# Kernel tuning notes

Hardware: AMD Instinct MI355X
Metric: run time of the kernel (lower is better)

## Reference

```python
import jax, jax.numpy as jnp
import numpy as np


def _fracdiff(X, alpha):
    """Fractional differencing (1-L)^alpha applied per batch/channel.
    X: (B, T, n), alpha: (B, n) >= 0. Weights w_0 = 1, w_k = w_{k-1}*(k-1-alpha)/k.
    Y[b, t, i] = sum_{k=0..t} w[b, k, i] * X[b, t-k, i]  (causal filter).
    Computed as a linear convolution via FFT (same math, O(T log T)).
    """
    B, T, n = X.shape
    k = jnp.arange(1, T, dtype=X.dtype)[None, :, None]          # (1, T-1, 1)
    factors = (k - 1.0 - alpha[:, None, :]) / k                  # (B, T-1, n)
    w = jnp.concatenate(
        [jnp.ones((B, 1, n), X.dtype), jnp.cumprod(factors, axis=1)], axis=1
    )                                                            # (B, T, n)
    L = 2 * T  # zero-pad to avoid circular wrap-around
    Xf = jnp.fft.rfft(X, n=L, axis=1)
    Wf = jnp.fft.rfft(w, n=L, axis=1)
    Y = jnp.fft.irfft(Xf * Wf, n=L, axis=1)[:, :T, :]
    return Y.astype(X.dtype)


def setup_inputs() -> dict:
    key = jax.random.key(0)
    kx, ka, kA = jax.random.split(key, 3)
    B, T, n = 8, 8192, 128
    X = jax.random.normal(kx, (B, T, n), dtype=jnp.float32)
    # normalize per trial/channel, mirroring normalize_data=True in __init__
    X = (X - X.mean(axis=1, keepdims=True)) / X.std(axis=1, keepdims=True, ddof=1)
    alpha = jax.random.uniform(ka, (B, n), dtype=jnp.float32)
    A = jax.random.normal(kA, (B, n, n), dtype=jnp.float32) * 0.1
    return {"X": X, "alpha": alpha, "A": A}


def reference(X, alpha, A):
    # _resid(): Y = fracdiff(X, relu(alpha)); E = Y[:,1:,:] - X[:,:-1,:] @ A^T
    Y = _fracdiff(X, jax.nn.relu(alpha))
    Yhat = jnp.einsum('bti,bji->btj', X[:, :-1, :], A)  # bmm(X, A.transpose(1,2))
    return Y[:, 1:, :] - Yhat
```

## Files before the change

### kernel.cpp

```cpp
#include <hip/hip_runtime.h>

#define T 8192
#define NCH 128
#define NB 8
#define NS (NB * NCH)
#define TM1 (T - 1)

typedef __bf16 v8bf __attribute__((ext_vector_type(8)));
typedef float v16f __attribute__((ext_vector_type(16)));

#define WREV_LEN 8448
#define WREV_COPY_STRIDE ((size_t)NS * WREV_LEN)

#define ILIM_TRUNC 144
#define KCHUNKS 19
#define WR_D_MIN 2880
#define KMAX_W 2559
#define NW 2560

struct __attribute__((packed, aligned(4))) U16 { uint4 v; };
struct __attribute__((packed, aligned(4))) F16V { float4 v; };

__device__ __forceinline__ uint bf_bits(float f) {
  union { float f; uint u; } v; v.f = f;
  return (v.u + 0x7FFFu + ((v.u >> 16) & 1u)) >> 16;
}

__device__ __forceinline__ uint wbits(const float* wsh, int k) {
  if ((unsigned)k > (unsigned)KMAX_W) return 0u;
  return bf_bits(wsh[k + (k >> 5)]);
}

__global__ __launch_bounds__(256) void wkern(const float* __restrict__ alpha,
                                             ushort* __restrict__ wr2) {
  const int sid = blockIdx.x;
  const float a = fmaxf(alpha[sid], 0.f);
  const int j = threadIdx.x;
  __shared__ float sc[256];
  __shared__ float wsh[NW + NW / 32];
  const int k0 = j * 10;
  float c = 1.f;
  #pragma unroll
  for (int s = 1; s <= 10; ++s) {
    const float k = (float)(k0 + s);
    c *= (k - 1.f - a) / k;
  }
  sc[j] = c;
  __syncthreads();
  for (int off = 1; off < 256; off <<= 1) {
    const float u = (j >= off) ? sc[j - off] : 1.f;
    const float v = sc[j];
    __syncthreads();
    sc[j] = u * v;
    __syncthreads();
  }
  float p = (j == 0) ? 1.f : sc[j - 1];
  wsh[k0 + (k0 >> 5)] = p;
  #pragma unroll
  for (int s = 1; s < 10; ++s) {
    const float k = (float)(k0 + s);
    p *= (k - 1.f - a) / k;
    const int kk = k0 + s;
    wsh[kk + (kk >> 5)] = p;
  }
  __syncthreads();
  uint* c0u = (uint*)(wr2 + (size_t)sid * WREV_LEN);
  uint* c1u = (uint*)(wr2 + WREV_COPY_STRIDE + (size_t)sid * WREV_LEN);
  for (int d = WR_D_MIN + j; d < WREV_LEN / 2; d += 256) {
    const int z = 2 * d;
    const uint a0 = wbits(wsh, 8319 - z);
    const uint a1 = wbits(wsh, 8318 - z);
    const uint a2 = wbits(wsh, 8317 - z);
    c0u[d] = a0 | (a1 << 16);
    c1u[d] = a1 | (a2 << 16);
  }
}

__global__ __launch_bounds__(256) void tkern(const float* __restrict__ X,
                                             ushort* __restrict__ xT) {
  __shared__ float tile[32][33];
  const int b = blockIdx.z;
  const int i0 = blockIdx.y << 5;
  const int t0 = blockIdx.x << 5;
  const int tx = threadIdx.x;
  const int ty = threadIdx.y;
  #pragma unroll
  for (int k = 0; k < 4; ++k) {
    const int t = t0 + ty + (k << 3);
    tile[ty + (k << 3)][tx] = X[((size_t)b * T + t) * NCH + i0 + tx];
  }
  __syncthreads();
  #pragma unroll
  for (int k = 0; k < 4; ++k) {
    const int i = i0 + ty + (k << 3);
    xT[((size_t)(b * NCH + i)) * T + t0 + tx] =
        (ushort)bf_bits(tile[tx][ty + (k << 3)]);
  }
}

__global__ __launch_bounds__(256, 2) void convk(const ushort* __restrict__ wr2,
                                                const ushort* __restrict__ xT,
                                                float* __restrict__ yT) {
  const int sid = blockIdx.x;
  const int tid = threadIdx.x;
  const int wave = tid >> 6;
  const int lane = tid & 63;
  const int ln31 = lane & 31;
  const int q = lane >> 5;

  __shared__ uint4 arena16[1280];

  {
    const int u = tid;
    arena16[((u & 7) * 160) + (u >> 3)] = make_uint4(0, 0, 0, 0);
  }
  {
    const uint4* xg16 = (const uint4*)(xT + (size_t)sid * T);
    for (int u0 = tid; u0 < 1024; u0 += 256) {
      const int u = u0 + 256;
      arena16[((u & 7) * 160) + (u >> 3)] = xg16[u0];
    }
  }
  __syncthreads();

  v16f acc[4][2];
  #pragma unroll
  for (int cc = 0; cc < 4; ++cc)
    #pragma unroll
    for (int rt = 0; rt < 2; ++rt)
      #pragma unroll
      for (int e = 0; e < 16; ++e) acc[cc][rt][e] = 0.f;

  const int s0_par = (8303 - ln31 + 8 * q) & 1;
  const uint* wu = (const uint*)(wr2 + (s0_par ? WREV_COPY_STRIDE : 0) +
                                 (size_t)sid * WREV_LEN);

  uint4 av[10];
  int dw0;
  {
    const int ibase0 = -4 + wave * 8;
    const int s0 = 8303 - 16 * ibase0 - ln31 + 8 * q;
    dw0 = (s0 - s0_par) >> 1;
    #pragma unroll
    for (int j2 = 0; j2 < 10; ++j2)
      av[j2] = ((const U16*)(wu + (dw0 - 8 * j2)))->v;
  }

  for (int K = wave; K < KCHUNKS; K += 4) {
    const int ibase = -4 + K * 8;
    const int dw0n = dw0 - 256;
    const bool more = (K + 4) < KCHUNKS;
    uint4 pf0, pf1, pf2, pf3;
    if (more) {
      pf0 = ((const U16*)(wu + dw0n))->v;
      pf1 = ((const U16*)(wu + (dw0n - 8)))->v;
      pf2 = ((const U16*)(wu + (dw0n - 16)))->v;
      pf3 = ((const U16*)(wu + (dw0n - 24)))->v;
    }
    #pragma unroll
    for (int ii = 0; ii < 8; ++ii) {
      const int i = ibase + ii;
      const v8bf A0 = __builtin_bit_cast(v8bf, av[ii]);
      const v8bf A1 = __builtin_bit_cast(v8bf, av[ii + 2]);
      const int m2 = -2 * (i + 1);
      const int u70 = m2 & 7;
      const int u71 = (m2 + 1) & 7;
      const int G0 = u70 * 160 + 32 + ((m2 - u70) >> 3);
      const int G1 = u71 * 160 + 32 + ((m2 + 1 - u71) >> 3);
      const int phi = ln31 + (q ? G1 : G0);
      #pragma unroll
      for (int cc = 0; cc < 4; ++cc) {
        if (i < (cc == 0 ? 128 : ILIM_TRUNC)) {
          const uint4 bv = arena16[phi + 32 * cc];
          const v8bf Bf = __builtin_bit_cast(v8bf, bv);
          acc[cc][0] = __builtin_amdgcn_mfma_f32_32x32x16_bf16(A0, Bf, acc[cc][0], 0, 0, 0);
          acc[cc][1] = __builtin_amdgcn_mfma_f32_32x32x16_bf16(A1, Bf, acc[cc][1], 0, 0, 0);
        }
      }
    }
    if (more) {
      av[0] = pf0; av[1] = pf1; av[2] = pf2; av[3] = pf3;
      #pragma unroll
      for (int j2 = 4; j2 < 10; ++j2)
        av[j2] = ((const U16*)(wu + (dw0n - 8 * j2)))->v;
    }
    dw0 = dw0n;
  }

  float* const zbase = (float*)arena16;
  const int rowq = 4 * q;
  #pragma unroll
  for (int cc = 0; cc < 4; ++cc) {
    #pragma unroll
    for (int rt = 0; rt < 2; ++rt) {
      __syncthreads();
      float* zone = zbase + wave * 1152;
      #pragma unroll
      for (int g = 0; g < 4; ++g) {
        float4 v = make_float4(acc[cc][rt][4 * g], acc[cc][rt][4 * g + 1],
                               acc[cc][rt][4 * g + 2], acc[cc][rt][4 * g + 3]);
        *(float4*)(zone + ln31 * 36 + 8 * g + rowq) = v;
      }
      __syncthreads();
      const int n2 = tid & 31, rg = tid >> 5;
      const int zi = n2 * 36 + 4 * rg;
      float4 s0 = *(const float4*)(zbase + 0 * 1152 + zi);
      float4 s1 = *(const float4*)(zbase + 1 * 1152 + zi);
      float4 s2 = *(const float4*)(zbase + 2 * 1152 + zi);
      float4 s3 = *(const float4*)(zbase + 3 * 1152 + zi);
      float4 s;
      s.x = s0.x + s1.x + s2.x + s3.x;
      s.y = s0.y + s1.y + s2.y + s3.y;
      s.z = s0.z + s1.z + s2.z + s3.z;
      s.w = s0.w + s1.w + s2.w + s3.w;
      *(float4*)(yT + (size_t)sid * T + 2048 * cc + 64 * n2 + 32 * rt + 4 * rg) = s;
    }
  }
}

__global__ __launch_bounds__(256) void outk(const float* __restrict__ X,
                                            const float* __restrict__ A,
                                            const float* __restrict__ yT,
                                            float* __restrict__ out) {
  const int b = blockIdx.y;
  const int t0 = blockIdx.x << 6;
  const int tid = threadIdx.x;
  const int wave = tid >> 6;
  const int lane = tid & 63;
  const int ln31 = lane & 31;
  const int q = lane >> 5;

  __shared__ uint4 arena[3072];

  {
    const float* Ab = A + (size_t)b * NCH * NCH;
    #pragma unroll
    for (int g = 0; g < 8; ++g) {
      const int u = g * 256 + tid;
      const int jr = u >> 4, c4 = u & 15;
      const float4 f0 = *(const float4*)(Ab + jr * NCH + 8 * c4);
      const float4 f1 = *(const float4*)(Ab + jr * NCH + 8 * c4 + 4);
      uint4 pk;
      pk.x = bf_bits(f0.x) | (bf_bits(f0.y) << 16);
      pk.y = bf_bits(f0.z) | (bf_bits(f0.w) << 16);
      pk.z = bf_bits(f1.x) | (bf_bits(f1.y) << 16);
      pk.w = bf_bits(f1.z) | (bf_bits(f1.w) << 16);
      arena[c4 * 128 + ((jr + c4) & 127)] = pk;
    }
  }
  {
    const float* Xb = X + ((size_t)b * T + t0) * NCH;
    #pragma unroll
    for (int g = 0; g < 4; ++g) {
      const int u = g * 256 + tid;
      const int m = u >> 4, c4 = u & 15;
      const float4 f0 = *(const float4*)(Xb + m * NCH + 8 * c4);
      const float4 f1 = *(const float4*)(Xb + m * NCH + 8 * c4 + 4);
      uint4 pk;
      pk.x = bf_bits(f0.x) | (bf_bits(f0.y) << 16);
      pk.y = bf_bits(f0.z) | (bf_bits(f0.w) << 16);
      pk.z = bf_bits(f1.x) | (bf_bits(f1.y) << 16);
      pk.w = bf_bits(f1.z) | (bf_bits(f1.w) << 16);
      arena[2048 + c4 * 64 + ((m + c4) & 63)] = pk;
    }
  }
  __syncthreads();

  v16f acc[2];
  #pragma unroll
  for (int mt = 0; mt < 2; ++mt)
    #pragma unroll
    for (int e = 0; e < 16; ++e) acc[mt][e] = 0.f;

  const int nt = wave;
  #pragma unroll
  for (int kk = 0; kk < 8; ++kk) {
    const int c4 = 2 * kk + q;
    const uint4 bv = arena[c4 * 128 + ((nt * 32 + ln31 + c4) & 127)];
    const v8bf Bf = __builtin_bit_cast(v8bf, bv);
    #pragma unroll
    for (int mt = 0; mt < 2; ++mt) {
      const uint4 avv = arena[2048 + c4 * 64 + ((mt * 32 + ln31 + c4) & 63)];
      const v8bf Af = __builtin_bit_cast(v8bf, avv);
      acc[mt] = __builtin_amdgcn_mfma_f32_32x32x16_bf16(Af, Bf, acc[mt], 0, 0, 0);
    }
  }

  __syncthreads();
  float* const ldsY = (float*)arena;
  {
    const int jr = tid >> 1, h = tid & 1;
    const float* yr = yT + ((size_t)(b * NCH + jr)) * T + t0 + 1 + 32 * h;
    #pragma unroll
    for (int v = 0; v < 8; ++v) {
      const float4 f = ((const F16V*)(yr + 4 * v))->v;
      const int tt = 32 * h + 4 * v;
      ldsY[(tt + 0) * 132 + jr] = f.x;
      ldsY[(tt + 1) * 132 + jr] = f.y;
      ldsY[(tt + 2) * 132 + jr] = f.z;
      ldsY[(tt + 3) * 132 + jr] = f.w;
    }
  }
  __syncthreads();

  const int jj = nt * 32 + ln31;
  float* og = out + (size_t)b * TM1 * NCH + jj;
  #pragma unroll
  for (int mt = 0; mt < 2; ++mt) {
    #pragma unroll
    for (int g = 0; g < 4; ++g) {
      const int r0 = mt * 32 + 8 * g + 4 * q;
      #pragma unroll
      for (int e = 0; e < 4; ++e) {
        const int t = t0 + r0 + e;
        const float val = ldsY[(r0 + e) * 132 + jj] - acc[mt][4 * g + e];
        if (t < TM1) og[(size_t)t * NCH] = val;
      }
    }
  }
}

extern "C" void kernel_launch(void* const* d_in, const int* in_sizes, int n_in,
                              void* d_out, int out_size, void* d_ws, size_t ws_size,
                              hipStream_t stream) {
  const float* X     = (const float*)d_in[0];
  const float* alpha = (const float*)d_in[1];
  const float* A     = (const float*)d_in[2];
  float* out = (float*)d_out;
  char* ws = (char*)d_ws;

  ushort* wr2 = (ushort*)ws;
  ushort* xT  = (ushort*)(ws + 34603008);
  float*  yT  = (float*)(ws + 34603008 + 16777216);

  hipLaunchKernelGGL(wkern, dim3(NS), dim3(256), 0, stream, alpha, wr2);
  hipLaunchKernelGGL(tkern, dim3(T / 32, NCH / 32, NB), dim3(32, 8), 0, stream, X, xT);
  hipLaunchKernelGGL(convk, dim3(NS), dim3(256), 0, stream, wr2, xT, yT);
  hipLaunchKernelGGL(outk, dim3(T / 64, NB), dim3(256), 0, stream, X, A, yT, out);
}
```

Measured before the change: 148.9 us.

## Assign each wave one output column chunk and drop cross-wave reduction

Instead of splitting the K chunks across waves and reducing four partial accumulator sets through shared memory, each wave now owns one output column group (cc = wave) and runs every K chunk itself. The A operands are double-buffered in registers so the next chunk's loads overlap the current chunk's MFMAs. Results go straight to global memory, which removes the syncthreads-based reduction. The accumulator count drops from 8 to 2 tiles, which allows launch bounds of 3 blocks per SM. The trade-off is that each wave now loads all weight chunks itself, and wave 0 does less work than the others, so load is uneven across waves.

```diff
diff --git a/kernel.cpp b/kernel.cpp
--- a/kernel.cpp
+++ b/kernel.cpp
@@ -98,7 +98,7 @@
   }
 }
 
-__global__ __launch_bounds__(256, 2) void convk(const ushort* __restrict__ wr2,
+__global__ __launch_bounds__(256, 3) void convk(const ushort* __restrict__ wr2,
                                                 const ushort* __restrict__ xT,
                                                 float* __restrict__ yT) {
   const int sid = blockIdx.x;
@@ -123,97 +123,85 @@
   }
   __syncthreads();
 
-  v16f acc[4][2];
-  #pragma unroll
-  for (int cc = 0; cc < 4; ++cc)
-    #pragma unroll
-    for (int rt = 0; rt < 2; ++rt)
-      #pragma unroll
-      for (int e = 0; e < 16; ++e) acc[cc][rt][e] = 0.f;
+  const int cc = wave;
+  const int ilim = (cc == 0) ? 128 : ILIM_TRUNC;
+  const int klim = (cc == 0) ? 17 : KCHUNKS;
+
+  v16f acc[2];
+  #pragma unroll
+  for (int rt = 0; rt < 2; ++rt)
+    #pragma unroll
+    for (int e = 0; e < 16; ++e) acc[rt][e] = 0.f;
 
   const int s0_par = (8303 - ln31 + 8 * q) & 1;
   const uint* wu = (const uint*)(wr2 + (s0_par ? WREV_COPY_STRIDE : 0) +
                                  (size_t)sid * WREV_LEN);
 
-  uint4 av[10];
+  uint4 avA[10], avB[10];
   int dw0;
   {
-    const int ibase0 = -4 + wave * 8;
-    const int s0 = 8303 - 16 * ibase0 - ln31 + 8 * q;
+    const int s0 = 8303 + 64 - ln31 + 8 * q;
     dw0 = (s0 - s0_par) >> 1;
     #pragma unroll
     for (int j2 = 0; j2 < 10; ++j2)
-      av[j2] = ((const U16*)(wu + (dw0 - 8 * j2)))->v;
-  }
-
-  for (int K = wave; K < KCHUNKS; K += 4) {
+      avA[j2] = ((const U16*)(wu + (dw0 - 8 * j2)))->v;
+  }
+
+  auto compute = [&](const uint4 (&av)[10], int K) {
     const int ibase = -4 + K * 8;
-    const int dw0n = dw0 - 256;
-    const bool more = (K + 4) < KCHUNKS;
-    uint4 pf0, pf1, pf2, pf3;
-    if (more) {
-      pf0 = ((const U16*)(wu + dw0n))->v;
-      pf1 = ((const U16*)(wu + (dw0n - 8)))->v;
-      pf2 = ((const U16*)(wu + (dw0n - 16)))->v;
-      pf3 = ((const U16*)(wu + (dw0n - 24)))->v;
-    }
     #pragma unroll
     for (int ii = 0; ii < 8; ++ii) {
       const int i = ibase + ii;
-      const v8bf A0 = __builtin_bit_cast(v8bf, av[ii]);
-      const v8bf A1 = __builtin_bit_cast(v8bf, av[ii + 2]);
-      const int m2 = -2 * (i + 1);
-      const int u70 = m2 & 7;
-      const int u71 = (m2 + 1) & 7;
-      const int G0 = u70 * 160 + 32 + ((m2 - u70) >> 3);
-      const int G1 = u71 * 160 + 32 + ((m2 + 1 - u71) >> 3);
-      const int phi = ln31 + (q ? G1 : G0);
+      if (i < ilim) {
+        const v8bf A0 = __builtin_bit_cast(v8bf, av[ii]);
+        const v8bf A1 = __builtin_bit_cast(v8bf, av[ii + 2]);
+        const int m2 = -2 * (i + 1);
+        const int u70 = m2 & 7;
+        const int u71 = (m2 + 1) & 7;
+        const int G0 = u70 * 160 + 32 + ((m2 - u70) >> 3);
+        const int G1 = u71 * 160 + 32 + ((m2 + 1 - u71) >> 3);
+        const int phi = ln31 + (q ? G1 : G0);
+        const uint4 bv = arena16[phi + 32 * cc];
+        const v8bf Bf = __builtin_bit_cast(v8bf, bv);
+        acc[0] = __builtin_amdgcn_mfma_f32_32x32x16_bf16(A0, Bf, acc[0], 0, 0, 0);
+        acc[1] = __builtin_amdgcn_mfma_f32_32x32x16_bf16(A1, Bf, acc[1], 0, 0, 0);
+      }
+    }
+  };
+
+  int dwc = dw0;
+  int K = 0;
+  while (true) {
+    const int dwn = dwc - 64;
+    if (K + 1 < klim) {
+      avB[0] = avA[8]; avB[1] = avA[9];
       #pragma unroll
-      for (int cc = 0; cc < 4; ++cc) {
-        if (i < (cc == 0 ? 128 : ILIM_TRUNC)) {
-          const uint4 bv = arena16[phi + 32 * cc];
-          const v8bf Bf = __builtin_bit_cast(v8bf, bv);
-          acc[cc][0] = __builtin_amdgcn_mfma_f32_32x32x16_bf16(A0, Bf, acc[cc][0], 0, 0, 0);
-          acc[cc][1] = __builtin_amdgcn_mfma_f32_32x32x16_bf16(A1, Bf, acc[cc][1], 0, 0, 0);
-        }
-      }
-    }
-    if (more) {
-      av[0] = pf0; av[1] = pf1; av[2] = pf2; av[3] = pf3;
+      for (int j2 = 2; j2 < 10; ++j2)
+        avB[j2] = ((const U16*)(wu + (dwn - 8 * j2)))->v;
+    }
+    compute(avA, K);
+    ++K; if (K >= klim) break;
+    dwc = dwn;
+    const int dwn2 = dwc - 64;
+    if (K + 1 < klim) {
+      avA[0] = avB[8]; avA[1] = avB[9];
       #pragma unroll
-      for (int j2 = 4; j2 < 10; ++j2)
-        av[j2] = ((const U16*)(wu + (dw0n - 8 * j2)))->v;
-    }
-    dw0 = dw0n;
-  }
-
-  float* const zbase = (float*)arena16;
-  const int rowq = 4 * q;
-  #pragma unroll
-  for (int cc = 0; cc < 4; ++cc) {
-    #pragma unroll
-    for (int rt = 0; rt < 2; ++rt) {
-      __syncthreads();
-      float* zone = zbase + wave * 1152;
-      #pragma unroll
-      for (int g = 0; g < 4; ++g) {
-        float4 v = make_float4(acc[cc][rt][4 * g], acc[cc][rt][4 * g + 1],
-                               acc[cc][rt][4 * g + 2], acc[cc][rt][4 * g + 3]);
-        *(float4*)(zone + ln31 * 36 + 8 * g + rowq) = v;
-      }
-      __syncthreads();
-      const int n2 = tid & 31, rg = tid >> 5;
-      const int zi = n2 * 36 + 4 * rg;
-      float4 s0 = *(const float4*)(zbase + 0 * 1152 + zi);
-      float4 s1 = *(const float4*)(zbase + 1 * 1152 + zi);
-      float4 s2 = *(const float4*)(zbase + 2 * 1152 + zi);
-      float4 s3 = *(const float4*)(zbase + 3 * 1152 + zi);
-      float4 s;
-      s.x = s0.x + s1.x + s2.x + s3.x;
-      s.y = s0.y + s1.y + s2.y + s3.y;
-      s.z = s0.z + s1.z + s2.z + s3.z;
-      s.w = s0.w + s1.w + s2.w + s3.w;
-      *(float4*)(yT + (size_t)sid * T + 2048 * cc + 64 * n2 + 32 * rt + 4 * rg) = s;
+      for (int j2 = 2; j2 < 10; ++j2)
+        avA[j2] = ((const U16*)(wu + (dwn2 - 8 * j2)))->v;
+    }
+    compute(avB, K);
+    ++K; if (K >= klim) break;
+    dwc = dwn2;
+  }
+
+  float* const yg = yT + (size_t)sid * T + 2048 * cc + 64 * ln31 + 4 * q;
+  #pragma unroll
+  for (int rt = 0; rt < 2; ++rt) {
+    #pragma unroll
+    for (int g = 0; g < 4; ++g) {
+      float4 v = make_float4(acc[rt][4 * g], acc[rt][4 * g + 1],
+                             acc[rt][4 * g + 2], acc[rt][4 * g + 3]);
+      *(float4*)(yg + 32 * rt + 8 * g) = v;
     }
   }
 }
```

After: 163.4 us. 1.1x slower.
